# Optimization experiments

Measured on AMD Instinct MI355X. Metric: run time of the kernel, lower is better.

The kernel has to match this reference:

```python
import jax, jax.numpy as jnp
import numpy as np

N_NODES = 50000
N_EDGES = 800000
IN_DIM = 89
HID = 128
N_CLASSES = 64
N_GRAPHS = 64


def setup_inputs() -> dict:
    key = jax.random.key(0)
    ks = jax.random.split(key, 12)
    nf = jax.random.normal(ks[0], (N_NODES, IN_DIM), dtype=jnp.float32)
    src = jax.random.randint(ks[1], (N_EDGES,), 0, N_NODES, dtype=jnp.int32)
    dst = jnp.sort(jax.random.randint(ks[2], (N_EDGES,), 0, N_NODES, dtype=jnp.int32))
    graph_id = jnp.sort(jax.random.randint(ks[3], (N_NODES,), 0, N_GRAPHS, dtype=jnp.int32))
    s = 0.05
    W1 = jax.random.normal(ks[4], (IN_DIM, HID), dtype=jnp.float32) * s
    b1 = jnp.zeros((HID,), jnp.float32)
    W2 = jax.random.normal(ks[5], (HID, HID), dtype=jnp.float32) * s
    b2 = jnp.zeros((HID,), jnp.float32)
    W3 = jax.random.normal(ks[6], (HID, HID), dtype=jnp.float32) * s
    b3 = jnp.zeros((HID,), jnp.float32)
    Wc1 = jax.random.normal(ks[7], (HID, HID), dtype=jnp.float32) * s
    bc1 = jnp.zeros((HID,), jnp.float32)
    Wc2 = jax.random.normal(ks[8], (HID, N_CLASSES), dtype=jnp.float32) * s
    bc2 = jnp.zeros((N_CLASSES,), jnp.float32)
    return {"nf": nf, "src": src, "dst": dst, "graph_id": graph_id,
            "n_graphs": N_GRAPHS,
            "W1": W1, "b1": b1, "W2": W2, "b2": b2, "W3": W3, "b3": b3,
            "Wc1": Wc1, "bc1": bc1, "Wc2": Wc2, "bc2": bc2}


def reference(nf, src, dst, graph_id, n_graphs, W1, b1, W2, b2, W3, b3, Wc1, bc1, Wc2, bc2):
    n = nf.shape[0]
    # in-degree per destination node (DGL mean over mailbox); clamp to avoid /0
    deg = jax.ops.segment_sum(jnp.ones((src.shape[0],), nf.dtype), dst, num_segments=n)
    inv_deg = (1.0 / jnp.maximum(deg, 1.0))[:, None]

    def gcn(h, W, b):
        # copy_u: gather source features per edge, mean-reduce by dst, linear+ReLU
        agg = jax.ops.segment_sum(h[src], dst, num_segments=n) * inv_deg
        return jax.nn.relu(agg @ W + b)

    h = gcn(nf, W1, b1)
    h = gcn(h, W2, b2)
    h = gcn(h, W3, b3)

    # dgl.mean_nodes: per-graph mean pool over nodes
    cnt = jax.ops.segment_sum(jnp.ones((n,), h.dtype), graph_id, num_segments=n_graphs)
    hg = jax.ops.segment_sum(h, graph_id, num_segments=n_graphs) / jnp.maximum(cnt, 1.0)[:, None]

    return jax.nn.relu(hg @ Wc1 + bc1) @ Wc2 + bc2
```

## Files before the change

### kernel.cpp

```cpp
#include <hip/hip_runtime.h>

#define N_NODES   50000
#define N_EDGES   800000
#define IN_DIM    89
#define KP1       96
#define HID       128
#define N_CLASSES 64
#define N_GRAPHS  64
#define PSPLIT    16

typedef __attribute__((ext_vector_type(8))) short bf16x8;
typedef __attribute__((ext_vector_type(4))) float f32x4;

__device__ __forceinline__ unsigned short f2bf(float x) {
    union { float f; unsigned u; } v; v.f = x;
    unsigned r = v.u + 0x7FFF + ((v.u >> 16) & 1);
    return (unsigned short)(r >> 16);
}
__device__ __forceinline__ float bf2f(unsigned short x) {
    union { unsigned u; float f; } v; v.u = ((unsigned)x) << 16;
    return v.f;
}

#define NB_ROW  196
#define NB_WT2  128
#define NB_PRE  (NB_ROW + NB_WT2)
#define GEMM1_GRID ((N_NODES + 63) / 64)
#define WS1 100

__global__ __launch_bounds__(256) void prep_gemm1_kernel(
        const int* __restrict__ dst,
        const int* __restrict__ gid,
        const float* __restrict__ W1,
        const float* __restrict__ W2,
        const float* __restrict__ W3,
        const float* __restrict__ nf,
        int* __restrict__ node_ptr,
        int* __restrict__ graph_ptr,
        unsigned short* __restrict__ wt2,
        unsigned short* __restrict__ wt3,
        unsigned short* __restrict__ Y) {
    __shared__ unsigned short wt1s[HID * WS1];

    const int b = blockIdx.x;
    if (b < NB_ROW) {
        const int i = b * 256 + threadIdx.x;
        if (i <= N_NODES) {
            int lo = 0, hi = N_EDGES;
            while (lo < hi) { int mid = (lo + hi) >> 1; if (dst[mid] < i) lo = mid + 1; else hi = mid; }
            node_ptr[i] = lo;
        }
        if (i <= N_GRAPHS) {
            int lo = 0, hi = N_NODES;
            while (lo < hi) { int mid = (lo + hi) >> 1; if (gid[mid] < i) lo = mid + 1; else hi = mid; }
            graph_ptr[i] = lo;
        }
        return;
    }
    if (b < NB_PRE) {
        int idx = (b - NB_ROW) * 256 + threadIdx.x;
        if (idx < HID * HID) {
            const int col = idx / HID, k = idx - col * HID;
            wt2[idx] = f2bf(W2[(size_t)k * HID + col]);
        } else {
            idx -= HID * HID;
            const int col = idx / HID, k = idx - col * HID;
            wt3[idx] = f2bf(W3[(size_t)k * HID + col]);
        }
        return;
    }

    const int tid = threadIdx.x;
    for (int idx = tid; idx < KP1 * HID; idx += 256) {
        const int k = idx >> 7, col = idx & 127;
        const float v = (k < IN_DIM) ? W1[(size_t)k * HID + col] : 0.f;
        wt1s[col * WS1 + k] = f2bf(v);
    }
    __syncthreads();

    const int wave = tid >> 6;
    const int lane = tid & 63;
    const int r    = lane & 15;
    const int kg   = lane >> 4;

    const int row  = (b - NB_PRE) * 64 + wave * 16 + r;
    const int rowc = (row < N_NODES) ? row : (N_NODES - 1);

    bf16x8 afrag[3];
#pragma unroll
    for (int t = 0; t < 3; ++t) {
        const int kb = 32 * t + kg * 8;
#pragma unroll
        for (int j = 0; j < 8; ++j) {
            const int k = kb + j;
            const float v = (k < IN_DIM) ? nf[(size_t)rowc * IN_DIM + k] : 0.f;
            afrag[t][j] = (short)f2bf(v);
        }
    }

    f32x4 acc[8];
#pragma unroll
    for (int i = 0; i < 8; ++i) acc[i] = (f32x4){0.f, 0.f, 0.f, 0.f};

#pragma unroll
    for (int t = 0; t < 3; ++t) {
#pragma unroll
        for (int c = 0; c < 8; ++c) {
            const bf16x8 bb = *reinterpret_cast<const bf16x8*>(
                &wt1s[(c * 16 + r) * WS1 + kg * 8 + 32 * t]);
            acc[c] = __builtin_amdgcn_mfma_f32_16x16x32_bf16(afrag[t], bb, acc[c], 0, 0, 0);
        }
    }

    const int orow0 = (b - NB_PRE) * 64 + wave * 16 + kg * 4;
#pragma unroll
    for (int c = 0; c < 8; ++c)
#pragma unroll
        for (int p = 0; p < 4; ++p) {
            const int orow = orow0 + p;
            if (orow < N_NODES) Y[(size_t)orow * HID + c * 16 + r] = f2bf(acc[c][p]);
        }
}

__global__ __launch_bounds__(256) void fused_agg_gemm_kernel(
        const unsigned short* __restrict__ Pin,
        const int* __restrict__ src,
        const int* __restrict__ node_ptr,
        const float* __restrict__ bias,
        const unsigned short* __restrict__ WT,
        unsigned short* __restrict__ Pout) {
    __shared__ unsigned short hs[16][136];
    __shared__ int cnt;

    const int tid  = threadIdx.x;
    const int lane = tid & 63;
    const int q    = lane >> 4;
    const int g    = lane & 15;
    const int vbase = blockIdx.x * 16;

    if (tid == 0) cnt = 0;
    __syncthreads();

    const float4 b0 = *reinterpret_cast<const float4*>(bias + g * 8);
    const float4 b1 = *reinterpret_cast<const float4*>(bias + g * 8 + 4);

    for (;;) {
        int li;
        if (lane == 0) li = atomicAdd(&cnt, 1);
        li = __shfl(li, 0);
        if (li >= 16) break;

        const int v  = vbase + li;
        const int lo = node_ptr[v];
        const int hi = node_ptr[v + 1];
        const float inv = 1.0f / (float)max(hi - lo, 1);

        float acc[8];
#pragma unroll
        for (int j = 0; j < 8; ++j) acc[j] = 0.f;

        int e = lo + q;
        for (; e + 12 < hi; e += 16) {
            const int u0 = src[e];
            const int u1 = src[e + 4];
            const int u2 = src[e + 8];
            const int u3 = src[e + 12];
            const bf16x8 r0 = *reinterpret_cast<const bf16x8*>(Pin + (size_t)u0 * HID + g * 8);
            const bf16x8 r1 = *reinterpret_cast<const bf16x8*>(Pin + (size_t)u1 * HID + g * 8);
            const bf16x8 r2 = *reinterpret_cast<const bf16x8*>(Pin + (size_t)u2 * HID + g * 8);
            const bf16x8 r3 = *reinterpret_cast<const bf16x8*>(Pin + (size_t)u3 * HID + g * 8);
#pragma unroll
            for (int j = 0; j < 8; ++j)
                acc[j] += (bf2f((unsigned short)r0[j]) + bf2f((unsigned short)r1[j]))
                        + (bf2f((unsigned short)r2[j]) + bf2f((unsigned short)r3[j]));
        }
        for (; e < hi; e += 4) {
            const int u = src[e];
            const bf16x8 r = *reinterpret_cast<const bf16x8*>(Pin + (size_t)u * HID + g * 8);
#pragma unroll
            for (int j = 0; j < 8; ++j) acc[j] += bf2f((unsigned short)r[j]);
        }
#pragma unroll
        for (int j = 0; j < 8; ++j) {
            acc[j] += __shfl_xor(acc[j], 16);
            acc[j] += __shfl_xor(acc[j], 32);
        }
        if (q == 0) {
            bf16x8 ob;
            ob[0] = (short)f2bf(fmaxf(acc[0] * inv + b0.x, 0.f));
            ob[1] = (short)f2bf(fmaxf(acc[1] * inv + b0.y, 0.f));
            ob[2] = (short)f2bf(fmaxf(acc[2] * inv + b0.z, 0.f));
            ob[3] = (short)f2bf(fmaxf(acc[3] * inv + b0.w, 0.f));
            ob[4] = (short)f2bf(fmaxf(acc[4] * inv + b1.x, 0.f));
            ob[5] = (short)f2bf(fmaxf(acc[5] * inv + b1.y, 0.f));
            ob[6] = (short)f2bf(fmaxf(acc[6] * inv + b1.z, 0.f));
            ob[7] = (short)f2bf(fmaxf(acc[7] * inv + b1.w, 0.f));
            *reinterpret_cast<bf16x8*>(&hs[li][g * 8]) = ob;
        }
    }
    __syncthreads();

    const int wave = tid >> 6;
    const int r  = lane & 15;
    const int kg = lane >> 4;

    f32x4 acc2[2];
#pragma unroll
    for (int t = 0; t < 2; ++t) acc2[t] = (f32x4){0.f, 0.f, 0.f, 0.f};

#pragma unroll
    for (int k0 = 0; k0 < HID; k0 += 32) {
        const bf16x8 a = *reinterpret_cast<const bf16x8*>(&hs[r][kg * 8 + k0]);
#pragma unroll
        for (int t = 0; t < 2; ++t) {
            const int nf = wave * 2 + t;
            const bf16x8 b = *reinterpret_cast<const bf16x8*>(
                WT + (size_t)(nf * 16 + r) * HID + kg * 8 + k0);
            acc2[t] = __builtin_amdgcn_mfma_f32_16x16x32_bf16(a, b, acc2[t], 0, 0, 0);
        }
    }

    const int orow0 = vbase + kg * 4;
#pragma unroll
    for (int t = 0; t < 2; ++t) {
        const int nf = wave * 2 + t;
#pragma unroll
        for (int p = 0; p < 4; ++p)
            Pout[(size_t)(orow0 + p) * HID + nf * 16 + r] = f2bf(acc2[t][p]);
    }
}

__global__ void agg128_f32_kernel(const unsigned short* __restrict__ Pb,
                                  const int* __restrict__ src,
                                  const int* __restrict__ node_ptr,
                                  const float* __restrict__ bias,
                                  float* __restrict__ out) {
    const int wave = threadIdx.x >> 6;
    const int lane = threadIdx.x & 63;
    const int v    = blockIdx.x * 4 + wave;
    if (v >= N_NODES) return;

    const int lo = node_ptr[v];
    const int hi = node_ptr[v + 1];
    const float inv = 1.0f / (float)max(hi - lo, 1);

    const int q = lane >> 4;
    const int g = lane & 15;

    float acc[8];
#pragma unroll
    for (int j = 0; j < 8; ++j) acc[j] = 0.f;

    int e = lo + q;
    for (; e + 12 < hi; e += 16) {
        const int u0 = src[e];
        const int u1 = src[e + 4];
        const int u2 = src[e + 8];
        const int u3 = src[e + 12];
        const bf16x8 r0 = *reinterpret_cast<const bf16x8*>(Pb + (size_t)u0 * HID + g * 8);
        const bf16x8 r1 = *reinterpret_cast<const bf16x8*>(Pb + (size_t)u1 * HID + g * 8);
        const bf16x8 r2 = *reinterpret_cast<const bf16x8*>(Pb + (size_t)u2 * HID + g * 8);
        const bf16x8 r3 = *reinterpret_cast<const bf16x8*>(Pb + (size_t)u3 * HID + g * 8);
#pragma unroll
        for (int j = 0; j < 8; ++j)
            acc[j] += (bf2f((unsigned short)r0[j]) + bf2f((unsigned short)r1[j]))
                    + (bf2f((unsigned short)r2[j]) + bf2f((unsigned short)r3[j]));
    }
    for (; e < hi; e += 4) {
        const int u = src[e];
        const bf16x8 r = *reinterpret_cast<const bf16x8*>(Pb + (size_t)u * HID + g * 8);
#pragma unroll
        for (int j = 0; j < 8; ++j) acc[j] += bf2f((unsigned short)r[j]);
    }
#pragma unroll
    for (int j = 0; j < 8; ++j) {
        acc[j] += __shfl_xor(acc[j], 16);
        acc[j] += __shfl_xor(acc[j], 32);
    }

    if (q == 0) {
        const float4 b0 = *reinterpret_cast<const float4*>(bias + g * 8);
        const float4 b1 = *reinterpret_cast<const float4*>(bias + g * 8 + 4);
        float4 a = make_float4(fmaxf(acc[0] * inv + b0.x, 0.f), fmaxf(acc[1] * inv + b0.y, 0.f),
                               fmaxf(acc[2] * inv + b0.z, 0.f), fmaxf(acc[3] * inv + b0.w, 0.f));
        float4 b = make_float4(fmaxf(acc[4] * inv + b1.x, 0.f), fmaxf(acc[5] * inv + b1.y, 0.f),
                               fmaxf(acc[6] * inv + b1.z, 0.f), fmaxf(acc[7] * inv + b1.w, 0.f));
        *reinterpret_cast<float4*>(out + (size_t)v * HID + g * 8)     = a;
        *reinterpret_cast<float4*>(out + (size_t)v * HID + g * 8 + 4) = b;
    }
}

__global__ void pool_partial_kernel(const float* __restrict__ h3,
                                    const int* __restrict__ graph_ptr,
                                    float* __restrict__ hgp) {
    const int g   = blockIdx.x / PSPLIT;
    const int s   = blockIdx.x % PSPLIT;
    const int j   = threadIdx.x;
    const int lo  = graph_ptr[g];
    const int hi  = graph_ptr[g + 1];

    float acc = 0.f;
    for (int r = lo + s; r < hi; r += PSPLIT)
        acc += h3[(size_t)r * HID + j];
    hgp[(size_t)blockIdx.x * HID + j] = acc;
}

__global__ void cls_kernel(const float* __restrict__ hgp,
                           const int* __restrict__ graph_ptr,
                           const float* __restrict__ Wc1,
                           const float* __restrict__ bc1,
                           const float* __restrict__ Wc2,
                           const float* __restrict__ bc2,
                           float* __restrict__ out) {
    const int g = blockIdx.x;
    const int j = threadIdx.x;
    const int cnt = graph_ptr[g + 1] - graph_ptr[g];
    const float inv = 1.0f / (float)max(cnt, 1);

    float acc = 0.f;
#pragma unroll
    for (int s = 0; s < PSPLIT; ++s)
        acc += hgp[(size_t)(g * PSPLIT + s) * HID + j];

    __shared__ float row[HID];
    __shared__ float trow[HID];
    row[j] = acc * inv;
    __syncthreads();

    float a1 = bc1[j];
#pragma unroll 4
    for (int k = 0; k < HID; ++k) a1 = fmaf(row[k], Wc1[k * HID + j], a1);
    trow[j] = fmaxf(a1, 0.f);
    __syncthreads();

    if (j < N_CLASSES) {
        float a2 = bc2[j];
#pragma unroll 4
        for (int k = 0; k < HID; ++k) a2 = fmaf(trow[k], Wc2[k * N_CLASSES + j], a2);
        out[g * N_CLASSES + j] = a2;
    }
}

extern "C" void kernel_launch(void* const* d_in, const int* in_sizes, int n_in,
                              void* d_out, int out_size, void* d_ws, size_t ws_size,
                              hipStream_t stream) {
    const float* nf   = (const float*)d_in[0];
    const int*   src  = (const int*)  d_in[1];
    const int*   dst  = (const int*)  d_in[2];
    const int*   gid  = (const int*)  d_in[3];
    const float* W1  = (const float*)d_in[5];
    const float* b1  = (const float*)d_in[6];
    const float* W2  = (const float*)d_in[7];
    const float* b2  = (const float*)d_in[8];
    const float* W3  = (const float*)d_in[9];
    const float* b3  = (const float*)d_in[10];
    const float* Wc1 = (const float*)d_in[11];
    const float* bc1 = (const float*)d_in[12];
    const float* Wc2 = (const float*)d_in[13];
    const float* bc2 = (const float*)d_in[14];
    float* out = (float*)d_out;

    char* ws = (char*)d_ws;
    size_t off = 0;
    auto alloc = [&](size_t bytes) { void* p = ws + off; off = (off + bytes + 255) & ~(size_t)255; return p; };
    int*   node_ptr  = (int*)  alloc((N_NODES + 1) * sizeof(int));
    int*   graph_ptr = (int*)  alloc((N_GRAPHS + 1) * sizeof(int));
    float* h3        = (float*)alloc((size_t)N_NODES * HID * sizeof(float));
    unsigned short* PbA = (unsigned short*)alloc((size_t)N_NODES * HID * sizeof(unsigned short));
    unsigned short* PbB = (unsigned short*)alloc((size_t)N_NODES * HID * sizeof(unsigned short));
    unsigned short* wt2 = (unsigned short*)alloc((size_t)HID * HID * sizeof(unsigned short));
    unsigned short* wt3 = (unsigned short*)alloc((size_t)HID * HID * sizeof(unsigned short));
    float* hgp       = (float*)alloc((size_t)N_GRAPHS * PSPLIT * HID * sizeof(float));
    (void)ws_size;

    const int FUSED_GRID = N_NODES / 16;
    const int AGG_GRID   = (N_NODES + 3) / 4;

    prep_gemm1_kernel<<<NB_PRE + GEMM1_GRID, 256, 0, stream>>>(
        dst, gid, W1, W2, W3, nf, node_ptr, graph_ptr, wt2, wt3, PbA);

    fused_agg_gemm_kernel<<<FUSED_GRID, 256, 0, stream>>>(PbA, src, node_ptr, b1, wt2, PbB);

    fused_agg_gemm_kernel<<<FUSED_GRID, 256, 0, stream>>>(PbB, src, node_ptr, b2, wt3, PbA);

    agg128_f32_kernel<<<AGG_GRID, 256, 0, stream>>>(PbA, src, node_ptr, b3, h3);

    pool_partial_kernel<<<N_GRAPHS * PSPLIT, HID, 0, stream>>>(h3, graph_ptr, hgp);
    cls_kernel<<<N_GRAPHS, HID, 0, stream>>>(hgp, graph_ptr, Wc1, bc1, Wc2, bc2, out);
}
```

Baseline: 177.3 us.

## Store projected features in 32-column panels and split aggregation from GEMM

Projected node features are now written in a panel-major layout of four 32-column slices, so each aggregation block gathers only 64-byte rows from one panel. Block order interleaves panels so that neighbouring blocks work on the same panel and can reuse cache. The goal is a smaller gather working set per pass and better L2 hit rates. The fused aggregate-plus-GEMM kernels are split into separate aggregation and MFMA GEMM launches, which adds kernel launches and an extra bf16 round trip of the hidden state through memory. Edge index loads now use nontemporal hints.

```diff
diff --git a/kernel.cpp b/kernel.cpp
--- a/kernel.cpp
+++ b/kernel.cpp
@@ -20,6 +20,10 @@
 __device__ __forceinline__ float bf2f(unsigned short x) {
     union { unsigned u; float f; } v; v.u = ((unsigned)x) << 16;
     return v.f;
+}
+
+__device__ __forceinline__ size_t pidx(int panel, int node, int off) {
+    return ((size_t)panel * N_NODES + node) * 32 + off;
 }
 
 #define NB_ROW  196
@@ -114,179 +118,139 @@
 
     const int orow0 = (b - NB_PRE) * 64 + wave * 16 + kg * 4;
 #pragma unroll
-    for (int c = 0; c < 8; ++c)
+    for (int c = 0; c < 8; ++c) {
+        const int col = c * 16 + r;
+        const int pan = col >> 5, off = col & 31;
 #pragma unroll
         for (int p = 0; p < 4; ++p) {
             const int orow = orow0 + p;
-            if (orow < N_NODES) Y[(size_t)orow * HID + c * 16 + r] = f2bf(acc[c][p]);
-        }
-}
-
-__global__ __launch_bounds__(256) void fused_agg_gemm_kernel(
-        const unsigned short* __restrict__ Pin,
+            if (orow < N_NODES) Y[pidx(pan, orow, off)] = f2bf(acc[c][p]);
+        }
+    }
+}
+
+template <bool OUT_F32>
+__global__ __launch_bounds__(256) void agg_panel_kernel(
+        const unsigned short* __restrict__ Pp,
         const int* __restrict__ src,
         const int* __restrict__ node_ptr,
         const float* __restrict__ bias,
-        const unsigned short* __restrict__ WT,
-        unsigned short* __restrict__ Pout) {
-    __shared__ unsigned short hs[16][136];
-    __shared__ int cnt;
-
-    const int tid  = threadIdx.x;
-    const int lane = tid & 63;
-    const int q    = lane >> 4;
-    const int g    = lane & 15;
-    const int vbase = blockIdx.x * 16;
-
-    if (tid == 0) cnt = 0;
-    __syncthreads();
-
-    const float4 b0 = *reinterpret_cast<const float4*>(bias + g * 8);
-    const float4 b1 = *reinterpret_cast<const float4*>(bias + g * 8 + 4);
-
-    for (;;) {
-        int li;
-        if (lane == 0) li = atomicAdd(&cnt, 1);
-        li = __shfl(li, 0);
-        if (li >= 16) break;
-
-        const int v  = vbase + li;
-        const int lo = node_ptr[v];
-        const int hi = node_ptr[v + 1];
-        const float inv = 1.0f / (float)max(hi - lo, 1);
-
-        float acc[8];
-#pragma unroll
-        for (int j = 0; j < 8; ++j) acc[j] = 0.f;
-
-        int e = lo + q;
-        for (; e + 12 < hi; e += 16) {
-            const int u0 = src[e];
-            const int u1 = src[e + 4];
-            const int u2 = src[e + 8];
-            const int u3 = src[e + 12];
-            const bf16x8 r0 = *reinterpret_cast<const bf16x8*>(Pin + (size_t)u0 * HID + g * 8);
-            const bf16x8 r1 = *reinterpret_cast<const bf16x8*>(Pin + (size_t)u1 * HID + g * 8);
-            const bf16x8 r2 = *reinterpret_cast<const bf16x8*>(Pin + (size_t)u2 * HID + g * 8);
-            const bf16x8 r3 = *reinterpret_cast<const bf16x8*>(Pin + (size_t)u3 * HID + g * 8);
-#pragma unroll
-            for (int j = 0; j < 8; ++j)
-                acc[j] += (bf2f((unsigned short)r0[j]) + bf2f((unsigned short)r1[j]))
-                        + (bf2f((unsigned short)r2[j]) + bf2f((unsigned short)r3[j]));
-        }
-        for (; e < hi; e += 4) {
-            const int u = src[e];
-            const bf16x8 r = *reinterpret_cast<const bf16x8*>(Pin + (size_t)u * HID + g * 8);
-#pragma unroll
-            for (int j = 0; j < 8; ++j) acc[j] += bf2f((unsigned short)r[j]);
-        }
-#pragma unroll
-        for (int j = 0; j < 8; ++j) {
-            acc[j] += __shfl_xor(acc[j], 16);
-            acc[j] += __shfl_xor(acc[j], 32);
-        }
-        if (q == 0) {
-            bf16x8 ob;
-            ob[0] = (short)f2bf(fmaxf(acc[0] * inv + b0.x, 0.f));
-            ob[1] = (short)f2bf(fmaxf(acc[1] * inv + b0.y, 0.f));
-            ob[2] = (short)f2bf(fmaxf(acc[2] * inv + b0.z, 0.f));
-            ob[3] = (short)f2bf(fmaxf(acc[3] * inv + b0.w, 0.f));
-            ob[4] = (short)f2bf(fmaxf(acc[4] * inv + b1.x, 0.f));
-            ob[5] = (short)f2bf(fmaxf(acc[5] * inv + b1.y, 0.f));
-            ob[6] = (short)f2bf(fmaxf(acc[6] * inv + b1.z, 0.f));
-            ob[7] = (short)f2bf(fmaxf(acc[7] * inv + b1.w, 0.f));
-            *reinterpret_cast<bf16x8*>(&hs[li][g * 8]) = ob;
-        }
-    }
-    __syncthreads();
-
-    const int wave = tid >> 6;
-    const int r  = lane & 15;
-    const int kg = lane >> 4;
-
-    f32x4 acc2[2];
-#pragma unroll
-    for (int t = 0; t < 2; ++t) acc2[t] = (f32x4){0.f, 0.f, 0.f, 0.f};
-
-#pragma unroll
-    for (int k0 = 0; k0 < HID; k0 += 32) {
-        const bf16x8 a = *reinterpret_cast<const bf16x8*>(&hs[r][kg * 8 + k0]);
-#pragma unroll
-        for (int t = 0; t < 2; ++t) {
-            const int nf = wave * 2 + t;
-            const bf16x8 b = *reinterpret_cast<const bf16x8*>(
-                WT + (size_t)(nf * 16 + r) * HID + kg * 8 + k0);
-            acc2[t] = __builtin_amdgcn_mfma_f32_16x16x32_bf16(a, b, acc2[t], 0, 0, 0);
-        }
-    }
-
-    const int orow0 = vbase + kg * 4;
-#pragma unroll
-    for (int t = 0; t < 2; ++t) {
-        const int nf = wave * 2 + t;
-#pragma unroll
-        for (int p = 0; p < 4; ++p)
-            Pout[(size_t)(orow0 + p) * HID + nf * 16 + r] = f2bf(acc2[t][p]);
-    }
-}
-
-__global__ void agg128_f32_kernel(const unsigned short* __restrict__ Pb,
-                                  const int* __restrict__ src,
-                                  const int* __restrict__ node_ptr,
-                                  const float* __restrict__ bias,
-                                  float* __restrict__ out) {
+        void* __restrict__ outp) {
+    const int b     = blockIdx.x;
+    const int panel = b & 3;
+    const int nb    = ((b >> 3) << 1) + ((b & 7) >> 2);
+
     const int wave = threadIdx.x >> 6;
     const int lane = threadIdx.x & 63;
-    const int v    = blockIdx.x * 4 + wave;
-    if (v >= N_NODES) return;
-
+    const int nq = lane >> 4;
+    const int es = (lane >> 2) & 3;
+    const int dq = lane & 3;
+
+    const int v  = nb * 16 + wave * 4 + nq;
     const int lo = node_ptr[v];
     const int hi = node_ptr[v + 1];
     const float inv = 1.0f / (float)max(hi - lo, 1);
-
-    const int q = lane >> 4;
-    const int g = lane & 15;
+    const int last = (hi > lo) ? (hi - 1) : 0;
+
+    const unsigned short* base = Pp + (size_t)panel * N_NODES * 32 + dq * 8;
 
     float acc[8];
 #pragma unroll
     for (int j = 0; j < 8; ++j) acc[j] = 0.f;
 
-    int e = lo + q;
+    int e = lo + es;
     for (; e + 12 < hi; e += 16) {
-        const int u0 = src[e];
-        const int u1 = src[e + 4];
-        const int u2 = src[e + 8];
-        const int u3 = src[e + 12];
-        const bf16x8 r0 = *reinterpret_cast<const bf16x8*>(Pb + (size_t)u0 * HID + g * 8);
-        const bf16x8 r1 = *reinterpret_cast<const bf16x8*>(Pb + (size_t)u1 * HID + g * 8);
-        const bf16x8 r2 = *reinterpret_cast<const bf16x8*>(Pb + (size_t)u2 * HID + g * 8);
-        const bf16x8 r3 = *reinterpret_cast<const bf16x8*>(Pb + (size_t)u3 * HID + g * 8);
+        const int u0 = __builtin_nontemporal_load(src + e);
+        const int u1 = __builtin_nontemporal_load(src + e + 4);
+        const int u2 = __builtin_nontemporal_load(src + e + 8);
+        const int u3 = __builtin_nontemporal_load(src + e + 12);
+        const bf16x8 r0 = *reinterpret_cast<const bf16x8*>(base + (size_t)u0 * 32);
+        const bf16x8 r1 = *reinterpret_cast<const bf16x8*>(base + (size_t)u1 * 32);
+        const bf16x8 r2 = *reinterpret_cast<const bf16x8*>(base + (size_t)u2 * 32);
+        const bf16x8 r3 = *reinterpret_cast<const bf16x8*>(base + (size_t)u3 * 32);
 #pragma unroll
         for (int j = 0; j < 8; ++j)
             acc[j] += (bf2f((unsigned short)r0[j]) + bf2f((unsigned short)r1[j]))
                     + (bf2f((unsigned short)r2[j]) + bf2f((unsigned short)r3[j]));
     }
     for (; e < hi; e += 4) {
-        const int u = src[e];
-        const bf16x8 r = *reinterpret_cast<const bf16x8*>(Pb + (size_t)u * HID + g * 8);
+        const int u = __builtin_nontemporal_load(src + min(e, last));
+        const bf16x8 r = *reinterpret_cast<const bf16x8*>(base + (size_t)u * 32);
 #pragma unroll
         for (int j = 0; j < 8; ++j) acc[j] += bf2f((unsigned short)r[j]);
     }
+
 #pragma unroll
     for (int j = 0; j < 8; ++j) {
-        acc[j] += __shfl_xor(acc[j], 16);
-        acc[j] += __shfl_xor(acc[j], 32);
-    }
-
-    if (q == 0) {
-        const float4 b0 = *reinterpret_cast<const float4*>(bias + g * 8);
-        const float4 b1 = *reinterpret_cast<const float4*>(bias + g * 8 + 4);
-        float4 a = make_float4(fmaxf(acc[0] * inv + b0.x, 0.f), fmaxf(acc[1] * inv + b0.y, 0.f),
-                               fmaxf(acc[2] * inv + b0.z, 0.f), fmaxf(acc[3] * inv + b0.w, 0.f));
-        float4 b = make_float4(fmaxf(acc[4] * inv + b1.x, 0.f), fmaxf(acc[5] * inv + b1.y, 0.f),
-                               fmaxf(acc[6] * inv + b1.z, 0.f), fmaxf(acc[7] * inv + b1.w, 0.f));
-        *reinterpret_cast<float4*>(out + (size_t)v * HID + g * 8)     = a;
-        *reinterpret_cast<float4*>(out + (size_t)v * HID + g * 8 + 4) = b;
+        acc[j] += __shfl_xor(acc[j], 4);
+        acc[j] += __shfl_xor(acc[j], 8);
+    }
+
+    if (es == 0) {
+        const int d0 = panel * 32 + dq * 8;
+        const float4 b0 = *reinterpret_cast<const float4*>(bias + d0);
+        const float4 b1 = *reinterpret_cast<const float4*>(bias + d0 + 4);
+        float o[8];
+        o[0] = fmaxf(acc[0] * inv + b0.x, 0.f);
+        o[1] = fmaxf(acc[1] * inv + b0.y, 0.f);
+        o[2] = fmaxf(acc[2] * inv + b0.z, 0.f);
+        o[3] = fmaxf(acc[3] * inv + b0.w, 0.f);
+        o[4] = fmaxf(acc[4] * inv + b1.x, 0.f);
+        o[5] = fmaxf(acc[5] * inv + b1.y, 0.f);
+        o[6] = fmaxf(acc[6] * inv + b1.z, 0.f);
+        o[7] = fmaxf(acc[7] * inv + b1.w, 0.f);
+        if (OUT_F32) {
+            float* op = (float*)outp + (size_t)v * HID + d0;
+            *reinterpret_cast<float4*>(op)     = make_float4(o[0], o[1], o[2], o[3]);
+            *reinterpret_cast<float4*>(op + 4) = make_float4(o[4], o[5], o[6], o[7]);
+        } else {
+            bf16x8 ob;
+#pragma unroll
+            for (int j = 0; j < 8; ++j) ob[j] = (short)f2bf(o[j]);
+            *reinterpret_cast<bf16x8*>((unsigned short*)outp + (size_t)v * HID + d0) = ob;
+        }
+    }
+}
+
+__global__ __launch_bounds__(256) void mfma_gemm_kernel(
+        const unsigned short* __restrict__ Xb,
+        const unsigned short* __restrict__ WT,
+        unsigned short* __restrict__ Y) {
+    const int wave = threadIdx.x >> 6;
+    const int lane = threadIdx.x & 63;
+    const int r    = lane & 15;
+    const int kg   = lane >> 4;
+
+    const int row  = blockIdx.x * 64 + wave * 16 + r;
+    const int rowc = (row < N_NODES) ? row : (N_NODES - 1);
+
+    f32x4 acc[8];
+#pragma unroll
+    for (int i = 0; i < 8; ++i) acc[i] = (f32x4){0.f, 0.f, 0.f, 0.f};
+
+    const unsigned short* xrow = Xb + (size_t)rowc * HID + kg * 8;
+
+#pragma unroll
+    for (int k0 = 0; k0 < HID; k0 += 32) {
+        const bf16x8 a = *reinterpret_cast<const bf16x8*>(xrow + k0);
+#pragma unroll
+        for (int c = 0; c < 8; ++c) {
+            const bf16x8 bb = *reinterpret_cast<const bf16x8*>(
+                WT + (size_t)(c * 16 + r) * HID + kg * 8 + k0);
+            acc[c] = __builtin_amdgcn_mfma_f32_16x16x32_bf16(a, bb, acc[c], 0, 0, 0);
+        }
+    }
+
+    const int orow0 = blockIdx.x * 64 + wave * 16 + kg * 4;
+#pragma unroll
+    for (int c = 0; c < 8; ++c) {
+        const int col = c * 16 + r;
+        const int pan = col >> 5, off = col & 31;
+#pragma unroll
+        for (int p = 0; p < 4; ++p) {
+            const int orow = orow0 + p;
+            if (orow < N_NODES) Y[pidx(pan, orow, off)] = f2bf(acc[c][p]);
+        }
     }
 }
 
@@ -367,23 +331,27 @@
     int*   graph_ptr = (int*)  alloc((N_GRAPHS + 1) * sizeof(int));
     float* h3        = (float*)alloc((size_t)N_NODES * HID * sizeof(float));
     unsigned short* PbA = (unsigned short*)alloc((size_t)N_NODES * HID * sizeof(unsigned short));
-    unsigned short* PbB = (unsigned short*)alloc((size_t)N_NODES * HID * sizeof(unsigned short));
+    unsigned short* hb  = (unsigned short*)alloc((size_t)N_NODES * HID * sizeof(unsigned short));
     unsigned short* wt2 = (unsigned short*)alloc((size_t)HID * HID * sizeof(unsigned short));
     unsigned short* wt3 = (unsigned short*)alloc((size_t)HID * HID * sizeof(unsigned short));
     float* hgp       = (float*)alloc((size_t)N_GRAPHS * PSPLIT * HID * sizeof(float));
     (void)ws_size;
 
-    const int FUSED_GRID = N_NODES / 16;
-    const int AGG_GRID   = (N_NODES + 3) / 4;
+    const int AGG_GRID  = 12500;
+    const int GEMM_GRID = (N_NODES + 63) / 64;
 
     prep_gemm1_kernel<<<NB_PRE + GEMM1_GRID, 256, 0, stream>>>(
         dst, gid, W1, W2, W3, nf, node_ptr, graph_ptr, wt2, wt3, PbA);
 
-    fused_agg_gemm_kernel<<<FUSED_GRID, 256, 0, stream>>>(PbA, src, node_ptr, b1, wt2, PbB);
-
-    fused_agg_gemm_kernel<<<FUSED_GRID, 256, 0, stream>>>(PbB, src, node_ptr, b2, wt3, PbA);
-
-    agg128_f32_kernel<<<AGG_GRID, 256, 0, stream>>>(PbA, src, node_ptr, b3, h3);
+    agg_panel_kernel<false><<<AGG_GRID, 256, 0, stream>>>(PbA, src, node_ptr, b1, hb);
+
+    mfma_gemm_kernel<<<GEMM_GRID, 256, 0, stream>>>(hb, wt2, PbA);
+
+    agg_panel_kernel<false><<<AGG_GRID, 256, 0, stream>>>(PbA, src, node_ptr, b2, hb);
+
+    mfma_gemm_kernel<<<GEMM_GRID, 256, 0, stream>>>(hb, wt3, PbA);
+
+    agg_panel_kernel<true><<<AGG_GRID, 256, 0, stream>>>(PbA, src, node_ptr, b3, h3);
 
     pool_partial_kernel<<<N_GRAPHS * PSPLIT, HID, 0, stream>>>(h3, graph_ptr, hgp);
     cls_kernel<<<N_GRAPHS, HID, 0, stream>>>(hgp, graph_ptr, Wc1, bc1, Wc2, bc2, out);
```

Measured after the change: 249.4 us. +40.7%, slower.
